# Kernel optimization log

Hardware: AMD Instinct MI355X
Metric: run time of the kernel (lower is better)

Reference implementation:

```python
import jax, jax.numpy as jnp
import numpy as np
from jax.ops import segment_sum

N_NODES = 10000
N_EDGES = 160000
IN_FEAT = 256
OUT_FEAT = 256
NUM_RELS = 16


def setup_inputs() -> dict:
    key = jax.random.key(0)
    ks = jax.random.split(key, 8)
    feat = jax.random.normal(ks[0], (N_NODES, IN_FEAT), dtype=jnp.float32)
    Wf = jax.random.normal(ks[1], (NUM_RELS, IN_FEAT, OUT_FEAT), dtype=jnp.float32)
    Wb = jax.random.normal(ks[2], (NUM_RELS, IN_FEAT, OUT_FEAT), dtype=jnp.float32)
    loop_weight = jax.random.normal(ks[3], (IN_FEAT, OUT_FEAT), dtype=jnp.float32)
    forward_bias = jnp.zeros((OUT_FEAT,), dtype=jnp.float32)
    backward_bias = jnp.zeros((OUT_FEAT,), dtype=jnp.float32)
    self_bias = jnp.zeros((OUT_FEAT,), dtype=jnp.float32)
    src = jax.random.randint(ks[4], (N_EDGES,), 0, N_NODES, dtype=jnp.int32)
    dst = jax.random.randint(ks[5], (N_EDGES,), 0, N_NODES, dtype=jnp.int32)
    etypes = jax.random.randint(ks[6], (N_EDGES,), 0, NUM_RELS, dtype=jnp.int32)
    return {
        "feat": feat, "Wf": Wf, "Wb": Wb, "loop_weight": loop_weight,
        "forward_bias": forward_bias, "backward_bias": backward_bias,
        "self_bias": self_bias, "src": src, "dst": dst, "etypes": etypes,
        "use_dis_weight": 0, "drop_out": 0,
    }


def _inv_degree(idx, n):
    # dgl.norm_by_dst: 1/in-degree, with inf (zero-degree) replaced by 0
    deg = segment_sum(jnp.ones(idx.shape[0], dtype=jnp.float32), idx, num_segments=n)
    return jnp.where(deg > 0, 1.0 / deg, 0.0)


def _typed_pass(feat, W, bias, src_idx, dst_idx, etypes, norm_per_edge, n):
    # Per-relation projection of all nodes (grouped GEMM as R dense GEMMs),
    # then gather per-edge by (etype, src) -- avoids [E,in,out] weight gather.
    proj = jnp.einsum('ni,rio->rno', feat, W)          # [R, N, out]
    m = proj[etypes, src_idx] + bias                   # [E, out]
    m = m * norm_per_edge[:, None]
    return segment_sum(m, dst_idx, num_segments=n)     # [N, out]


def reference(feat, Wf, Wb, loop_weight, forward_bias, backward_bias,
              self_bias, src, dst, etypes, use_dis_weight, drop_out):
    n = feat.shape[0]
    # forward graph: messages src -> dst, norm by dst in-degree
    norm_f = _inv_degree(dst, n)[dst]                  # [E]
    m_forward = _typed_pass(feat, Wf, forward_bias, src, dst, etypes, norm_f, n)
    # reversed graph: src'=dst, dst'=src, same etype; norm by reversed dst in-degree
    norm_b = _inv_degree(src, n)[src]                  # [E]
    m_backward = _typed_pass(feat, Wb, backward_bias, dst, src, etypes, norm_b, n)
    # self loop (drop_out=False); faithful quirk: s += s + self_bias -> 2s + bias
    s = feat @ loop_weight
    s = s + s + self_bias
    return s + m_forward + m_backward
```

## Files before the change

kernel.cpp:

```cpp
#include <hip/hip_runtime.h>
#include <hip/hip_bf16.h>
#include <stdint.h>

#define N_NODES 10000
#define N_EDGES 160000
#define FEAT    256
#define NRELS   16
#define BM      64
#define NCHUNK  32
#define KBYTES  512

typedef __attribute__((ext_vector_type(8))) short bf16x8;
typedef __attribute__((ext_vector_type(4))) float f32x4;

__device__ __forceinline__ unsigned short f2bf(float f) {
    union { float f; unsigned u; } v; v.f = f;
    unsigned u = v.u;
    u += 0x7FFFu + ((u >> 16) & 1u);
    return (unsigned short)(u >> 16);
}
__device__ __forceinline__ float bf2f(unsigned short u) {
    union { unsigned u; float f; } v; v.u = ((unsigned)u) << 16;
    return v.f;
}

__global__ __launch_bounds__(256) void k_prep(const float4* __restrict__ src4,
                                              ushort4* __restrict__ dst4, int n4,
                                              const int* __restrict__ src,
                                              const int* __restrict__ dst,
                                              int* degd, int* degs) {
    int i = blockIdx.x * 256 + threadIdx.x;
    if (i < n4) {
        float4 v = src4[i];
        ushort4 r;
        r.x = f2bf(v.x); r.y = f2bf(v.y); r.z = f2bf(v.z); r.w = f2bf(v.w);
        dst4[i] = r;
    }
    if (i < N_EDGES) {
        atomicAdd(&degd[dst[i]], 1);
        atomicAdd(&degs[src[i]], 1);
    }
}

__global__ __launch_bounds__(256) void k_wtall(const float* __restrict__ Wf,
                                               const float* __restrict__ Wb,
                                               const float* __restrict__ lw,
                                               unsigned short* __restrict__ wall,
                                               unsigned short* __restrict__ lwt) {
    __shared__ float tile[64][65];
    int z = blockIdx.z;
    const float* w;
    unsigned short* o;
    if (z < 16)      { w = Wf + (size_t)z * 65536;        o = wall + (size_t)(z * 2) * 65536; }
    else if (z < 32) { w = Wb + (size_t)(z - 16) * 65536; o = wall + (size_t)((z - 16) * 2 + 1) * 65536; }
    else             { w = lw;                            o = lwt; }
    int i0 = blockIdx.x * 64, o0 = blockIdx.y * 64;
    int t = threadIdx.x;
    int c = t & 63, q = t >> 6;
#pragma unroll
    for (int it = 0; it < 16; it++) {
        int i = it * 4 + q;
        tile[i][c] = w[(size_t)(i0 + i) * 256 + o0 + c];
    }
    __syncthreads();
#pragma unroll
    for (int it = 0; it < 16; it++) {
        int oo = it * 4 + q;
        o[(size_t)(o0 + oo) * 256 + i0 + c] = f2bf(tile[c][oo]);
    }
}

__global__ __launch_bounds__(256) void k_off(const int* __restrict__ degd,
                                             const int* __restrict__ degs,
                                             int* offf, int* offb,
                                             int* curf, int* curb,
                                             float* normf, float* normb,
                                             int* gcnt) {
    __shared__ int sf[256], sb[256];
    __shared__ int basef, baseb;
    int t = threadIdx.x;
    int n = blockIdx.x * 256 + t;
    int df = (n < N_NODES) ? degd[n] : 0;
    int db = (n < N_NODES) ? degs[n] : 0;
    sf[t] = df; sb[t] = db;
    __syncthreads();
    for (int d = 1; d < 256; d <<= 1) {
        int vf = (t >= d) ? sf[t - d] : 0;
        int vb = (t >= d) ? sb[t - d] : 0;
        __syncthreads();
        sf[t] += vf; sb[t] += vb;
        __syncthreads();
    }
    if (t == 255) {
        basef = atomicAdd(&gcnt[0], sf[255]);
        baseb = atomicAdd(&gcnt[1], sb[255]);
    }
    __syncthreads();
    if (n < N_NODES) {
        int ef = basef + sf[t] - df;
        int eb = baseb + sb[t] - db;
        offf[n] = ef; offb[n] = eb;
        curf[n] = ef; curb[n] = eb;
        normf[n] = df > 0 ? 1.f / (float)df : 0.f;
        normb[n] = db > 0 ? 1.f / (float)db : 0.f;
    }
}

__global__ __launch_bounds__(256) void k_fill(const int* __restrict__ et,
                                              const int* __restrict__ src,
                                              const int* __restrict__ dst,
                                              int* curf, int* curb,
                                              int* csrf, int* csrb) {
    int e = blockIdx.x * 256 + threadIdx.x;
    if (e < N_EDGES) {
        int s = src[e], d = dst[e], r = et[e];
        csrf[atomicAdd(&curf[d], 1)] = s * NCHUNK + r * 2;
        csrb[atomicAdd(&curb[s], 1)] = d * NCHUNK + r * 2 + 1;
    }
}

__global__ __launch_bounds__(256) void k_self(const unsigned short* __restrict__ featb,
                                              const unsigned short* __restrict__ lwt,
                                              const float* __restrict__ sbias,
                                              float* __restrict__ out) {
    int m0 = blockIdx.x * BM;
    int wave = threadIdx.x >> 6, lane = threadIdx.x & 63;
    int nb = wave * 64, lr = lane & 15, lg = lane >> 4;
    f32x4 acc[4][4] = {};
    for (int k0 = 0; k0 < FEAT; k0 += 32) {
        int kk = k0 + lg * 8;
        bf16x8 a[4], b[4];
        for (int mi = 0; mi < 4; mi++) {
            int row = m0 + mi * 16 + lr;
            if (row >= N_NODES) row = N_NODES - 1;
            a[mi] = *(const bf16x8*)(featb + row * FEAT + kk);
        }
        for (int ni = 0; ni < 4; ni++) {
            int col = nb + ni * 16 + lr;
            b[ni] = *(const bf16x8*)(lwt + col * FEAT + kk);
        }
        for (int mi = 0; mi < 4; mi++)
            for (int ni = 0; ni < 4; ni++)
                acc[mi][ni] = __builtin_amdgcn_mfma_f32_16x16x32_bf16(a[mi], b[ni], acc[mi][ni], 0, 0, 0);
    }
    for (int mi = 0; mi < 4; mi++) {
        for (int j = 0; j < 4; j++) {
            int row = m0 + mi * 16 + lg * 4 + j;
            if (row < N_NODES) {
                for (int ni = 0; ni < 4; ni++) {
                    int col = nb + ni * 16 + lr;
                    out[row * FEAT + col] = 2.0f * acc[mi][ni][j] + sbias[col];
                }
            }
        }
    }
}

__global__ __launch_bounds__(256) void k_proj(const unsigned short* __restrict__ featb,
                                              const unsigned short* __restrict__ wall,
                                              unsigned short* __restrict__ proj) {
    __shared__ __align__(16) char lds[BM * KBYTES];
    int rd = blockIdx.x;
    int m0 = blockIdx.y * BM;
    int t = threadIdx.x;
    int wave = t >> 6, lane = t & 63;
    int nb = wave * 64, lr = lane & 15, lg = lane >> 4;
    const unsigned short* wr = wall + (size_t)rd * 256 * FEAT;

    {
        int rl = t >> 5;
        int kb = (t & 31) << 4;
#pragma unroll
        for (int it = 0; it < 8; it++) {
            int row = it * 8 + rl;
            int gr = m0 + row; if (gr > N_NODES - 1) gr = N_NODES - 1;
            bf16x8 v = *(const bf16x8*)(featb + gr * FEAT + (kb >> 1));
            *(bf16x8*)(lds + row * KBYTES + (kb ^ ((row & 7) << 4))) = v;
        }
    }
    __syncthreads();

    f32x4 acc[4][4] = {};
#pragma unroll 2
    for (int k0 = 0; k0 < FEAT; k0 += 32) {
        int kb = (k0 + lg * 8) * 2;
        bf16x8 a[4], b[4];
        for (int ni = 0; ni < 4; ni++)
            b[ni] = *(const bf16x8*)(wr + (nb + ni * 16 + lr) * FEAT + k0 + lg * 8);
        for (int mi = 0; mi < 4; mi++) {
            int row = mi * 16 + lr;
            a[mi] = *(const bf16x8*)(lds + row * KBYTES + (kb ^ ((row & 7) << 4)));
        }
        for (int mi = 0; mi < 4; mi++)
            for (int ni = 0; ni < 4; ni++)
                acc[mi][ni] = __builtin_amdgcn_mfma_f32_16x16x32_bf16(a[mi], b[ni], acc[mi][ni], 0, 0, 0);
    }
    __syncthreads();

    for (int mi = 0; mi < 4; mi++) {
#pragma unroll
        for (int j = 0; j < 4; j++) {
            int row = mi * 16 + lg * 4 + j;
            for (int ni = 0; ni < 4; ni++)
                *(unsigned short*)(lds + row * KBYTES + (nb + ni * 16 + lr) * 2) =
                    f2bf(acc[mi][ni][j]);
        }
    }
    __syncthreads();

    {
        int rl = t >> 5;
        int kb = (t & 31) << 4;
#pragma unroll
        for (int it = 0; it < 8; it++) {
            int row = it * 8 + rl;
            int gr = m0 + row;
            if (gr < N_NODES)
                *(bf16x8*)(proj + ((size_t)gr * NCHUNK + rd) * FEAT + (kb >> 1)) =
                    *(const bf16x8*)(lds + row * KBYTES + kb);
        }
    }
}

__global__ __launch_bounds__(256) void k_reduce(const unsigned short* __restrict__ proj,
                                                const int* __restrict__ csrf,
                                                const int* __restrict__ csrb,
                                                const int* __restrict__ offf,
                                                const int* __restrict__ offb,
                                                const int* __restrict__ degd,
                                                const int* __restrict__ degs,
                                                const float* __restrict__ normf,
                                                const float* __restrict__ normb,
                                                const float* __restrict__ biasf,
                                                const float* __restrict__ biasb,
                                                float* __restrict__ out) {
    int node = blockIdx.x * 4 + (threadIdx.x >> 6);
    if (node >= N_NODES) return;
    int lane = threadIdx.x & 63;
    int half = lane >> 5;
    int li = lane & 31;

    float af[8] = {0,0,0,0,0,0,0,0};
    float ab[8] = {0,0,0,0,0,0,0,0};

    int b0 = offf[node], dfc = degd[node];
    int b1 = b0 + dfc;
#pragma unroll 4
    for (int s = b0 + half; s < b1; s += 2) {
        int c = csrf[s];
        bf16x8 m = *(const bf16x8*)(proj + (size_t)c * FEAT + li * 8);
#pragma unroll
        for (int k = 0; k < 8; k++) af[k] += bf2f((unsigned short)m[k]);
    }
    int c0 = offb[node], dbc = degs[node];
    int c1 = c0 + dbc;
#pragma unroll 4
    for (int s = c0 + half; s < c1; s += 2) {
        int c = csrb[s];
        bf16x8 m = *(const bf16x8*)(proj + (size_t)c * FEAT + li * 8);
#pragma unroll
        for (int k = 0; k < 8; k++) ab[k] += bf2f((unsigned short)m[k]);
    }

    float nf = normf[node], nbv = normb[node];
    float v[8];
#pragma unroll
    for (int k = 0; k < 8; k++) v[k] = nf * af[k] + nbv * ab[k];
#pragma unroll
    for (int k = 0; k < 8; k++) v[k] += __shfl_xor(v[k], 32);

    int col = li * 8 + half * 4;
    float4 bfv = *(const float4*)(biasf + col);
    float4 bbv = *(const float4*)(biasb + col);
    float fb = (dfc > 0) ? 1.f : 0.f;
    float bb = (dbc > 0) ? 1.f : 0.f;
    float4 o = *(float4*)(out + (size_t)node * FEAT + col);
    int k0 = half * 4;
    o.x += v[k0 + 0] + fb * bfv.x + bb * bbv.x;
    o.y += v[k0 + 1] + fb * bfv.y + bb * bbv.y;
    o.z += v[k0 + 2] + fb * bfv.z + bb * bbv.z;
    o.w += v[k0 + 3] + fb * bfv.w + bb * bbv.w;
    *(float4*)(out + (size_t)node * FEAT + col) = o;
}

extern "C" void kernel_launch(void* const* d_in, const int* in_sizes, int n_in,
                              void* d_out, int out_size, void* d_ws, size_t ws_size,
                              hipStream_t stream) {
    const float* feat  = (const float*)d_in[0];
    const float* Wf    = (const float*)d_in[1];
    const float* Wb    = (const float*)d_in[2];
    const float* lw    = (const float*)d_in[3];
    const float* fbias = (const float*)d_in[4];
    const float* bbias = (const float*)d_in[5];
    const float* sbias = (const float*)d_in[6];
    const int*   src   = (const int*)d_in[7];
    const int*   dst   = (const int*)d_in[8];
    const int*   et    = (const int*)d_in[9];
    float* out = (float*)d_out;

    char* ws = (char*)d_ws;
    size_t off = 0;
    auto alloc = [&](size_t bytes) { void* p = ws + off; off = (off + bytes + 255) & ~(size_t)255; return p; };

    int*   degd  = (int*)alloc(N_NODES * 4);
    int*   degs  = (int*)alloc(N_NODES * 4);
    int*   gcnt  = (int*)alloc(64);
    size_t zero_bytes = off;
    int*   offf  = (int*)alloc(N_NODES * 4);
    int*   offb  = (int*)alloc(N_NODES * 4);
    int*   curf  = (int*)alloc(N_NODES * 4);
    int*   curb  = (int*)alloc(N_NODES * 4);
    float* normf = (float*)alloc(N_NODES * 4);
    float* normb = (float*)alloc(N_NODES * 4);
    int*   csrf  = (int*)alloc(N_EDGES * 4);
    int*   csrb  = (int*)alloc(N_EDGES * 4);
    unsigned short* featb = (unsigned short*)alloc((size_t)N_NODES * FEAT * 2);
    unsigned short* wall  = (unsigned short*)alloc((size_t)NCHUNK * 256 * FEAT * 2);
    unsigned short* lwt   = (unsigned short*)alloc((size_t)FEAT * FEAT * 2);
    unsigned short* proj  = (unsigned short*)alloc((size_t)N_NODES * NCHUNK * FEAT * 2);
    (void)ws_size;

    hipMemsetAsync(d_ws, 0, zero_bytes, stream);

    {
        int n4 = N_NODES * FEAT / 4;
        k_prep<<<(n4 + 255) / 256, 256, 0, stream>>>((const float4*)feat, (ushort4*)featb, n4,
                                                     src, dst, degd, degs);
    }
    {
        dim3 gw(4, 4, 33);
        k_wtall<<<gw, 256, 0, stream>>>(Wf, Wb, lw, wall, lwt);
    }
    k_off<<<(N_NODES + 255) / 256, 256, 0, stream>>>(degd, degs, offf, offb, curf, curb,
                                                     normf, normb, gcnt);
    k_fill<<<(N_EDGES + 255) / 256, 256, 0, stream>>>(et, src, dst, curf, curb, csrf, csrb);

    k_self<<<(N_NODES + BM - 1) / BM, 256, 0, stream>>>(featb, lwt, sbias, out);

    {
        dim3 grid(NCHUNK, (N_NODES + BM - 1) / BM);
        k_proj<<<grid, 256, 0, stream>>>(featb, wall, proj);
    }

    k_reduce<<<(N_NODES + 3) / 4, 256, 0, stream>>>(proj, csrf, csrb, offf, offb,
                                                    degd, degs, normf, normb,
                                                    fbias, bbias, out);
}
```

Before: 187.9 us.

## Merge self-loop GEMM into projection launch and load A tile via global_load_lds

Folds the self-loop GEMM kernel into the projection kernel as extra grid rows (5 extra y rows covering all 157 tiles), removing one launch and letting self tiles overlap with projection tiles. The A-tile staging into LDS now uses direct global-to-LDS 16-byte loads with the XOR swizzle applied on the source address instead of register round-trips. The reduce kernel's gather loops are unrolled by 8 instead of 4 for more memory-level parallelism. The fused kernel declares LDS that self tiles never use, which may lower their occupancy, and the swizzled global_load_lds addressing must line up with the per-wave LDS destination layout.

```diff
diff --git a/kernel.cpp b/kernel.cpp
--- a/kernel.cpp
+++ b/kernel.cpp
@@ -8,10 +8,17 @@
 #define NRELS   16
 #define BM      64
 #define NCHUNK  32
+#define NTILES  157
+#define SELFY   5
 #define KBYTES  512
 
 typedef __attribute__((ext_vector_type(8))) short bf16x8;
 typedef __attribute__((ext_vector_type(4))) float f32x4;
+
+#define GLL16(gsrc, ldst) \
+    __builtin_amdgcn_global_load_lds( \
+        (const __attribute__((address_space(1))) void*)(gsrc), \
+        (__attribute__((address_space(3))) void*)(ldst), 16, 0, 0)
 
 __device__ __forceinline__ unsigned short f2bf(float f) {
     union { float f; unsigned u; } v; v.f = f;
@@ -119,63 +126,67 @@
     }
 }
 
-__global__ __launch_bounds__(256) void k_self(const unsigned short* __restrict__ featb,
+__global__ __launch_bounds__(256) void k_proj(const unsigned short* __restrict__ featb,
+                                              const unsigned short* __restrict__ wall,
                                               const unsigned short* __restrict__ lwt,
                                               const float* __restrict__ sbias,
+                                              unsigned short* __restrict__ proj,
                                               float* __restrict__ out) {
-    int m0 = blockIdx.x * BM;
-    int wave = threadIdx.x >> 6, lane = threadIdx.x & 63;
-    int nb = wave * 64, lr = lane & 15, lg = lane >> 4;
-    f32x4 acc[4][4] = {};
-    for (int k0 = 0; k0 < FEAT; k0 += 32) {
-        int kk = k0 + lg * 8;
-        bf16x8 a[4], b[4];
-        for (int mi = 0; mi < 4; mi++) {
-            int row = m0 + mi * 16 + lr;
-            if (row >= N_NODES) row = N_NODES - 1;
-            a[mi] = *(const bf16x8*)(featb + row * FEAT + kk);
-        }
-        for (int ni = 0; ni < 4; ni++) {
-            int col = nb + ni * 16 + lr;
-            b[ni] = *(const bf16x8*)(lwt + col * FEAT + kk);
-        }
-        for (int mi = 0; mi < 4; mi++)
-            for (int ni = 0; ni < 4; ni++)
-                acc[mi][ni] = __builtin_amdgcn_mfma_f32_16x16x32_bf16(a[mi], b[ni], acc[mi][ni], 0, 0, 0);
-    }
-    for (int mi = 0; mi < 4; mi++) {
-        for (int j = 0; j < 4; j++) {
-            int row = m0 + mi * 16 + lg * 4 + j;
-            if (row < N_NODES) {
-                for (int ni = 0; ni < 4; ni++) {
-                    int col = nb + ni * 16 + lr;
-                    out[row * FEAT + col] = 2.0f * acc[mi][ni][j] + sbias[col];
-                }
-            }
-        }
-    }
-}
-
-__global__ __launch_bounds__(256) void k_proj(const unsigned short* __restrict__ featb,
-                                              const unsigned short* __restrict__ wall,
-                                              unsigned short* __restrict__ proj) {
     __shared__ __align__(16) char lds[BM * KBYTES];
     int rd = blockIdx.x;
-    int m0 = blockIdx.y * BM;
+    int y  = blockIdx.y;
     int t = threadIdx.x;
     int wave = t >> 6, lane = t & 63;
     int nb = wave * 64, lr = lane & 15, lg = lane >> 4;
+
+    if (y >= NTILES) {
+        int st = (y - NTILES) * NCHUNK + rd;
+        if (st >= NTILES) return;
+        int m0 = st * BM;
+        f32x4 acc[4][4] = {};
+        for (int k0 = 0; k0 < FEAT; k0 += 32) {
+            int kk = k0 + lg * 8;
+            bf16x8 a[4], b[4];
+            for (int mi = 0; mi < 4; mi++) {
+                int row = m0 + mi * 16 + lr;
+                if (row >= N_NODES) row = N_NODES - 1;
+                a[mi] = *(const bf16x8*)(featb + row * FEAT + kk);
+            }
+            for (int ni = 0; ni < 4; ni++)
+                b[ni] = *(const bf16x8*)(lwt + (nb + ni * 16 + lr) * FEAT + kk);
+            for (int mi = 0; mi < 4; mi++)
+                for (int ni = 0; ni < 4; ni++)
+                    acc[mi][ni] = __builtin_amdgcn_mfma_f32_16x16x32_bf16(a[mi], b[ni], acc[mi][ni], 0, 0, 0);
+        }
+        for (int mi = 0; mi < 4; mi++) {
+#pragma unroll
+            for (int j = 0; j < 4; j++) {
+                int row = m0 + mi * 16 + lg * 4 + j;
+                if (row < N_NODES) {
+                    for (int ni = 0; ni < 4; ni++) {
+                        int col = nb + ni * 16 + lr;
+                        out[(size_t)row * FEAT + col] = 2.0f * acc[mi][ni][j] + sbias[col];
+                    }
+                }
+            }
+        }
+        return;
+    }
+
+    int m0 = y * BM;
     const unsigned short* wr = wall + (size_t)rd * 256 * FEAT;
 
     {
-        int rl = t >> 5;
-        int kb = (t & 31) << 4;
+        int rbase = 2 * wave;
+        int rofs = lane >> 5;
+        int within = (lane & 31) << 4;
 #pragma unroll
         for (int it = 0; it < 8; it++) {
-            int row = it * 8 + rl;
+            int row = it * 8 + rbase + rofs;
             int gr = m0 + row; if (gr > N_NODES - 1) gr = N_NODES - 1;
-            bf16x8 v = *(const bf16x8*)(featb + gr * FEAT + (kb >> 1));
-            *(bf16x8*)(lds + row * KBYTES + (kb ^ ((row & 7) << 4))) = v;
+            const char* gsrc = (const char*)featb + (size_t)gr * KBYTES
+                               + (within ^ ((row & 7) << 4));
+            GLL16(gsrc, lds + (it * 8 + rbase) * KBYTES);
         }
     }
     __syncthreads();
@@ -245,7 +256,7 @@
 
     int b0 = offf[node], dfc = degd[node];
     int b1 = b0 + dfc;
-#pragma unroll 4
+#pragma unroll 8
     for (int s = b0 + half; s < b1; s += 2) {
         int c = csrf[s];
         bf16x8 m = *(const bf16x8*)(proj + (size_t)c * FEAT + li * 8);
@@ -254,7 +265,7 @@
     }
     int c0 = offb[node], dbc = degs[node];
     int c1 = c0 + dbc;
-#pragma unroll 4
+#pragma unroll 8
     for (int s = c0 + half; s < c1; s += 2) {
         int c = csrb[s];
         bf16x8 m = *(const bf16x8*)(proj + (size_t)c * FEAT + li * 8);
@@ -335,11 +346,9 @@
                                                      normf, normb, gcnt);
     k_fill<<<(N_EDGES + 255) / 256, 256, 0, stream>>>(et, src, dst, curf, curb, csrf, csrb);
 
-    k_self<<<(N_NODES + BM - 1) / BM, 256, 0, stream>>>(featb, lwt, sbias, out);
-
-    {
-        dim3 grid(NCHUNK, (N_NODES + BM - 1) / BM);
-        k_proj<<<grid, 256, 0, stream>>>(featb, wall, proj);
+    {
+        dim3 grid(NCHUNK, NTILES + SELFY);
+        k_proj<<<grid, 256, 0, stream>>>(featb, wall, lwt, sbias, proj, out);
     }
 
     k_reduce<<<(N_NODES + 3) / 4, 256, 0, stream>>>(proj, csrf, csrb, offf, offb,
```

Result: no change. 189.2 us (+0.7%).
